# Optimization experiments

Hardware: AMD Instinct MI355X
Metric: run time of the kernel (lower is better)

The kernel has to match this reference:

```python
import jax, jax.numpy as jnp
import numpy as np

NUM_EXPERTS = 256
TOP_K = 8
N_GROUP = 8
TOPK_GROUP = 4
ROUTED_SCALING = 2.5
HIDDEN = 7168
TOKENS = 16384


def setup_inputs() -> dict:
    key = jax.random.key(0)
    k1, k2, k3 = jax.random.split(key, 3)
    hidden_states = jax.random.normal(k1, (TOKENS, HIDDEN), dtype=jnp.float32)
    weight = jax.random.normal(k2, (NUM_EXPERTS, HIDDEN), dtype=jnp.float32) * 0.02
    e_score_correction_bias = jax.random.normal(k3, (NUM_EXPERTS,), dtype=jnp.float32) * 0.1
    return {
        "hidden_states": hidden_states,
        "weight": weight,
        "e_score_correction_bias": e_score_correction_bias,
    }


def reference(hidden_states, weight, e_score_correction_bias):
    T = hidden_states.shape[0]
    experts_per_group = NUM_EXPERTS // N_GROUP
    # Router logits: [T, num_experts]
    router_logits = jnp.einsum("th,eh->te", hidden_states.astype(jnp.float32), weight)
    scores = jax.nn.sigmoid(router_logits)
    scores_for_choice = scores + e_score_correction_bias  # broadcast over tokens
    # ---- group-limited top-k selection (noaux_tc) ----
    scores_grouped = scores_for_choice.reshape(T, N_GROUP, experts_per_group)
    group_top2, _ = jax.lax.top_k(scores_grouped, 2)           # [T, n_group, 2]
    group_scores = group_top2.sum(axis=-1)                      # [T, n_group]
    _, group_indices = jax.lax.top_k(group_scores, TOPK_GROUP)  # [T, topk_group]
    group_mask = jax.nn.one_hot(group_indices, N_GROUP, dtype=scores.dtype).max(axis=1)  # [T, n_group]
    expert_mask = jnp.broadcast_to(group_mask[:, :, None], (T, N_GROUP, experts_per_group)).reshape(T, NUM_EXPERTS)
    masked_scores = scores_for_choice * expert_mask
    # ---- final expert top-k ----
    _, selected_experts = jax.lax.top_k(masked_scores, TOP_K)   # [T, top_k]
    routing_weights = jnp.take_along_axis(scores, selected_experts, axis=-1)
    # norm_topk_prob
    routing_weights = routing_weights / (routing_weights.sum(axis=-1, keepdims=True) + 1e-20)
    routing_weights = routing_weights * ROUTED_SCALING
    return routing_weights, selected_experts
```

## Files before the change

kernel.cpp:

```cpp
#include <hip/hip_runtime.h>
#include <math.h>
#include <stdint.h>

#define TOKENS 16384
#define HIDDEN 7168
#define NE     256
#define NGROUP 8
#define GSIZE  32
#define TOPKG  4
#define TOPK   8

#define KSPLIT 2
#define TM     64
#define BK     32
#define KC_TOTAL (HIDDEN / BK)
#define KC_SLICE (KC_TOTAL / KSPLIT)

#define WPLANES_BYTES ((size_t)KC_TOTAL * 32 * 1024)

typedef _Float16 half8 __attribute__((ext_vector_type(8)));
typedef float    floatx4 __attribute__((ext_vector_type(4)));
typedef unsigned int u32;
#define GAS __attribute__((address_space(1)))
#define LAS __attribute__((address_space(3)))

__global__ void prep_w(const float* __restrict__ W, _Float16* __restrict__ wp) {
    const int c = blockIdx.x * 128 + threadIdx.x;
    const int e = blockIdx.y;
    const float* src = W + (size_t)e * HIDDEN + c * 8;
    float4 v0 = *(const float4*)src;
    float4 v1 = *(const float4*)(src + 4);
    float xv[8] = {v0.x, v0.y, v0.z, v0.w, v1.x, v1.y, v1.z, v1.w};
    half8 h, l;
    #pragma unroll
    for (int j = 0; j < 8; j++) {
        _Float16 hh = (_Float16)xv[j];
        h[j] = hh;
        l[j] = (_Float16)((xv[j] - (float)hh) * 2048.0f);
    }
    const int kc = c >> 2;
    const int g  = c & 3;
    const int lane = g * 16 + (e & 15);
    const int et   = e >> 4;
    const size_t base = (size_t)kc * 16384 + (size_t)et * 512 + (size_t)lane * 8;
    *(half8*)(wp + base)        = h;
    *(half8*)(wp + base + 8192) = l;
}

__global__ __launch_bounds__(256, 2)
void gemm_kernel(const float* __restrict__ X, const _Float16* __restrict__ wp,
                 float* __restrict__ partial) {
    __shared__ __align__(16) _Float16 smem[20480];

    const int tid  = threadIdx.x;
    const int b    = blockIdx.x;
    const int tb   = b >> 1;
    const int ks   = b & 1;
    const int t0   = tb * TM;

    const int w    = tid >> 6;
    const int lane = tid & 63;

    const int at = tid >> 2;
    const int ac = tid & 3;
    const int awoff = (at >> 4) * 512 + (ac * 16 + (at & 15)) * 8;
    const float* Xrow = X + (size_t)(t0 + at) * HIDDEN + ks * (HIDDEN / KSPLIT) + ac * 8;

    const char* wbase = (const char*)wp + (size_t)ks * KC_SLICE * 32768;

    floatx4 acc0[4][4], acc1[4][4];
    #pragma unroll
    for (int i = 0; i < 4; i++)
        #pragma unroll
        for (int j = 0; j < 4; j++) {
            acc0[i][j] = (floatx4){0.f, 0.f, 0.f, 0.f};
            acc1[i][j] = (floatx4){0.f, 0.f, 0.f, 0.f};
        }

    float4 v0 = *(const float4*)Xrow;
    float4 v1 = *(const float4*)(Xrow + 4);

    for (int i = 0; i < KC_SLICE; i++) {
        __syncthreads();

        {
            float xv[8] = {v0.x, v0.y, v0.z, v0.w, v1.x, v1.y, v1.z, v1.w};
            half8 ahh, ahl;
            #pragma unroll
            for (int j = 0; j < 8; j++) {
                _Float16 hh = (_Float16)xv[j];
                ahh[j] = hh;
                ahl[j] = (_Float16)((xv[j] - (float)hh) * 2048.0f);
            }
            *(half8*)(smem + awoff)        = ahh;
            *(half8*)(smem + 2048 + awoff) = ahl;
        }

        {
            const char* wsrc = wbase + (size_t)i * 32768;
            char* bdst = (char*)(smem + 4096);
            #pragma unroll
            for (int q = 0; q < 8; q++) {
                const int o = (tid + 256 * q) * 16;
                __builtin_amdgcn_global_load_lds((GAS const u32*)(wsrc + o),
                                                 (LAS u32*)(bdst + o), 16, 0, 0);
            }
        }

        __syncthreads();

        if (i + 1 < KC_SLICE) {
            const float* xp = Xrow + (size_t)(i + 1) * BK;
            v0 = *(const float4*)xp;
            v1 = *(const float4*)(xp + 4);
        }

        const _Float16* Bb = smem + 4096 + w * 2048;
        half8 bh[4], bl[4];
        #pragma unroll
        for (int et = 0; et < 4; et++) {
            bh[et] = *(const half8*)(Bb + et * 512 + lane * 8);
            bl[et] = *(const half8*)(Bb + 8192 + et * 512 + lane * 8);
        }
        #pragma unroll
        for (int mt = 0; mt < 4; mt++) {
            half8 ah = *(const half8*)(smem + mt * 512 + lane * 8);
            half8 al = *(const half8*)(smem + 2048 + mt * 512 + lane * 8);
            #pragma unroll
            for (int et = 0; et < 4; et++)
                acc0[mt][et] = __builtin_amdgcn_mfma_f32_16x16x32_f16(ah, bh[et], acc0[mt][et], 0, 0, 0);
            #pragma unroll
            for (int et = 0; et < 4; et++)
                acc1[mt][et] = __builtin_amdgcn_mfma_f32_16x16x32_f16(ah, bl[et], acc1[mt][et], 0, 0, 0);
            #pragma unroll
            for (int et = 0; et < 4; et++)
                acc1[mt][et] = __builtin_amdgcn_mfma_f32_16x16x32_f16(al, bh[et], acc1[mt][et], 0, 0, 0);
        }
    }

    float* P = partial + (size_t)ks * TOKENS * NE;
    const float inv = 1.0f / 2048.0f;
    #pragma unroll
    for (int mt = 0; mt < 4; mt++)
        #pragma unroll
        for (int et = 0; et < 4; et++) {
            floatx4 r = acc0[mt][et] + acc1[mt][et] * inv;
            const int col = w * 64 + 16 * et + (lane & 15);
            const int row = t0 + 16 * mt + (lane >> 4) * 4;
            #pragma unroll
            for (int rr = 0; rr < 4; rr++)
                P[(size_t)(row + rr) * NE + col] = r[rr];
        }
}

__global__ __launch_bounds__(256)
void select_kernel(const float* __restrict__ partial, const float* __restrict__ bias,
                   float* __restrict__ out) {
    __shared__ float sfc[32][257];
    const int tid = threadIdx.x;
    const int t0  = blockIdx.x * 32;
    const float* P0 = partial;
    const float* P1 = partial + (size_t)TOKENS * NE;

    for (int idx = tid; idx < 32 * NE; idx += 256) {
        const int t = idx >> 8;
        const int e = idx & 255;
        const size_t g = (size_t)(t0 + t) * NE + e;
        const float logit = P0[g] + P1[g];
        const float sig = 1.0f / (1.0f + expf(-logit));
        sfc[t][e] = sig + bias[e];
    }
    __syncthreads();

    if (tid < 32) {
        float* s = sfc[tid];
        float gs[NGROUP];
        #pragma unroll
        for (int g = 0; g < NGROUP; g++) {
            float m1 = -INFINITY, m2 = -INFINITY;
            for (int x = 0; x < GSIZE; x++) {
                const float v = s[g * GSIZE + x];
                if (v > m1) { m2 = m1; m1 = v; }
                else if (v > m2) { m2 = v; }
            }
            gs[g] = m1 + m2;
        }
        bool gsel[NGROUP] = {false,false,false,false,false,false,false,false};
        for (int r = 0; r < TOPKG; r++) {
            int bi = 0; float bv = -INFINITY;
            for (int g = 0; g < NGROUP; g++)
                if (!gsel[g] && gs[g] > bv) { bv = gs[g]; bi = g; }
            gsel[bi] = true;
        }
        int sel[TOPK]; float wgt[TOPK]; float sum = 0.f;
        for (int r = 0; r < TOPK; r++) {
            int bi = 0; float bv = -INFINITY;
            for (int e = 0; e < NE; e++) {
                const float sv = s[e];
                const float v = (sv == -INFINITY) ? -INFINITY
                               : (gsel[e >> 5] ? sv : 0.0f);
                if (v > bv) { bv = v; bi = e; }
            }
            sel[r] = bi;
            wgt[r] = s[bi] - bias[bi];
            s[bi]  = -INFINITY;
            sum += wgt[r];
        }
        const float scale = 2.5f / (sum + 1e-20f);
        const int gt = t0 + tid;
        #pragma unroll
        for (int r = 0; r < TOPK; r++) {
            out[(size_t)gt * TOPK + r] = wgt[r] * scale;
            out[(size_t)TOKENS * TOPK + (size_t)gt * TOPK + r] = (float)sel[r];
        }
    }
}

extern "C" void kernel_launch(void* const* d_in, const int* in_sizes, int n_in,
                              void* d_out, int out_size, void* d_ws, size_t ws_size,
                              hipStream_t stream) {
    const float* X  = (const float*)d_in[0];
    const float* W  = (const float*)d_in[1];
    const float* eb = (const float*)d_in[2];
    float* out = (float*)d_out;

    _Float16* wp   = (_Float16*)d_ws;
    float* partial = (float*)((char*)d_ws + WPLANES_BYTES);

    hipLaunchKernelGGL(prep_w, dim3(7, 256), dim3(128), 0, stream, W, wp);
    hipLaunchKernelGGL(gemm_kernel, dim3(TOKENS / TM * KSPLIT), dim3(256), 0, stream, X, wp, partial);
    hipLaunchKernelGGL(select_kernel, dim3(TOKENS / 32), dim3(256), 0, stream, partial, eb, out);
}
```

Baseline: 784.3 us.

## Double-buffer weight tiles, raise K-split to 4, warp-parallel routing selection

The GEMM now double-buffers the weight tiles in LDS, prefetching the next K chunk with global_load_lds while the current one is computed, and uses raw barriers with explicit waitcnt. KSPLIT doubles to 4, giving more blocks per token tile, and LDS grows to hold two weight buffers. The select kernel is rewritten so each wavefront handles one token, using shuffle reductions for group top-2, group ranking and the top-8 experts, in place of a single serial thread per token. The cost is more partial-sum traffic, larger LDS per block (which may limit occupancy), and hand-written waitcnt logic that must stay correct.

```diff
diff --git a/kernel.cpp b/kernel.cpp
--- a/kernel.cpp
+++ b/kernel.cpp
@@ -10,7 +10,7 @@
 #define TOPKG  4
 #define TOPK   8
 
-#define KSPLIT 2
+#define KSPLIT 4
 #define TM     64
 #define BK     32
 #define KC_TOTAL (HIDDEN / BK)
@@ -50,12 +50,12 @@
 __global__ __launch_bounds__(256, 2)
 void gemm_kernel(const float* __restrict__ X, const _Float16* __restrict__ wp,
                  float* __restrict__ partial) {
-    __shared__ __align__(16) _Float16 smem[20480];
+    __shared__ __align__(16) _Float16 smem[36864];
 
     const int tid  = threadIdx.x;
     const int b    = blockIdx.x;
-    const int tb   = b >> 1;
-    const int ks   = b & 1;
+    const int tb   = b >> 2;
+    const int ks   = b & 3;
     const int t0   = tb * TM;
 
     const int w    = tid >> 6;
@@ -77,11 +77,34 @@
             acc1[i][j] = (floatx4){0.f, 0.f, 0.f, 0.f};
         }
 
+    {
+        const char* wsrc = wbase;
+        char* bdst = (char*)(smem + 4096);
+        #pragma unroll
+        for (int q = 0; q < 8; q++) {
+            const int o = (tid + 256 * q) * 16;
+            __builtin_amdgcn_global_load_lds((GAS const u32*)(wsrc + o),
+                                             (LAS u32*)(bdst + o), 16, 0, 0);
+        }
+    }
     float4 v0 = *(const float4*)Xrow;
     float4 v1 = *(const float4*)(Xrow + 4);
 
     for (int i = 0; i < KC_SLICE; i++) {
-        __syncthreads();
+        const int cur = i & 1;
+
+        asm volatile("s_barrier" ::: "memory");
+
+        if (i + 1 < KC_SLICE) {
+            const char* wsrc = wbase + (size_t)(i + 1) * 32768;
+            char* bdst = (char*)(smem + 4096 + (cur ^ 1) * 16384);
+            #pragma unroll
+            for (int q = 0; q < 8; q++) {
+                const int o = (tid + 256 * q) * 16;
+                __builtin_amdgcn_global_load_lds((GAS const u32*)(wsrc + o),
+                                                 (LAS u32*)(bdst + o), 16, 0, 0);
+            }
+        }
 
         {
             float xv[8] = {v0.x, v0.y, v0.z, v0.w, v1.x, v1.y, v1.z, v1.w};
@@ -96,26 +119,20 @@
             *(half8*)(smem + 2048 + awoff) = ahl;
         }
 
-        {
-            const char* wsrc = wbase + (size_t)i * 32768;
-            char* bdst = (char*)(smem + 4096);
-            #pragma unroll
-            for (int q = 0; q < 8; q++) {
-                const int o = (tid + 256 * q) * 16;
-                __builtin_amdgcn_global_load_lds((GAS const u32*)(wsrc + o),
-                                                 (LAS u32*)(bdst + o), 16, 0, 0);
-            }
-        }
-
-        __syncthreads();
-
         if (i + 1 < KC_SLICE) {
+            asm volatile("s_waitcnt vmcnt(8) lgkmcnt(0)" ::: "memory");
+            __builtin_amdgcn_sched_barrier(0);
             const float* xp = Xrow + (size_t)(i + 1) * BK;
             v0 = *(const float4*)xp;
             v1 = *(const float4*)(xp + 4);
-        }
-
-        const _Float16* Bb = smem + 4096 + w * 2048;
+        } else {
+            asm volatile("s_waitcnt vmcnt(0) lgkmcnt(0)" ::: "memory");
+            __builtin_amdgcn_sched_barrier(0);
+        }
+
+        asm volatile("s_barrier" ::: "memory");
+
+        const _Float16* Bb = smem + 4096 + cur * 16384 + w * 2048;
         half8 bh[4], bl[4];
         #pragma unroll
         for (int et = 0; et < 4; et++) {
@@ -156,62 +173,85 @@
 __global__ __launch_bounds__(256)
 void select_kernel(const float* __restrict__ partial, const float* __restrict__ bias,
                    float* __restrict__ out) {
-    __shared__ float sfc[32][257];
-    const int tid = threadIdx.x;
-    const int t0  = blockIdx.x * 32;
-    const float* P0 = partial;
-    const float* P1 = partial + (size_t)TOKENS * NE;
-
-    for (int idx = tid; idx < 32 * NE; idx += 256) {
-        const int t = idx >> 8;
-        const int e = idx & 255;
-        const size_t g = (size_t)(t0 + t) * NE + e;
-        const float logit = P0[g] + P1[g];
-        const float sig = 1.0f / (1.0f + expf(-logit));
-        sfc[t][e] = sig + bias[e];
-    }
-    __syncthreads();
-
-    if (tid < 32) {
-        float* s = sfc[tid];
-        float gs[NGROUP];
-        #pragma unroll
-        for (int g = 0; g < NGROUP; g++) {
-            float m1 = -INFINITY, m2 = -INFINITY;
-            for (int x = 0; x < GSIZE; x++) {
-                const float v = s[g * GSIZE + x];
-                if (v > m1) { m2 = m1; m1 = v; }
-                else if (v > m2) { m2 = v; }
-            }
-            gs[g] = m1 + m2;
-        }
-        bool gsel[NGROUP] = {false,false,false,false,false,false,false,false};
-        for (int r = 0; r < TOPKG; r++) {
-            int bi = 0; float bv = -INFINITY;
-            for (int g = 0; g < NGROUP; g++)
-                if (!gsel[g] && gs[g] > bv) { bv = gs[g]; bi = g; }
-            gsel[bi] = true;
-        }
-        int sel[TOPK]; float wgt[TOPK]; float sum = 0.f;
+    const int lane = threadIdx.x & 63;
+    const int t    = blockIdx.x * 4 + (threadIdx.x >> 6);
+    const int e0   = lane * 4;
+
+    float lg[4] = {0.f, 0.f, 0.f, 0.f};
+    #pragma unroll
+    for (int s = 0; s < KSPLIT; s++) {
+        float4 p = *(const float4*)(partial + ((size_t)s * TOKENS + t) * NE + e0);
+        lg[0] += p.x; lg[1] += p.y; lg[2] += p.z; lg[3] += p.w;
+    }
+    float4 b4 = *(const float4*)(bias + e0);
+    const float bb[4] = {b4.x, b4.y, b4.z, b4.w};
+
+    float sig[4], sfc[4];
+    #pragma unroll
+    for (int j = 0; j < 4; j++) {
+        sig[j] = 1.0f / (1.0f + expf(-lg[j]));
+        sfc[j] = sig[j] + bb[j];
+    }
+
+    float m1 = sfc[0], m2 = -INFINITY;
+    #pragma unroll
+    for (int j = 1; j < 4; j++) {
+        if (sfc[j] > m1)      { m2 = m1; m1 = sfc[j]; }
+        else if (sfc[j] > m2) { m2 = sfc[j]; }
+    }
+    #pragma unroll
+    for (int d = 1; d < 8; d <<= 1) {
+        float o1 = __shfl_xor(m1, d);
+        float o2 = __shfl_xor(m2, d);
+        float hi = fmaxf(m1, o1);
+        float lo = fmaxf(fminf(m1, o1), fmaxf(m2, o2));
+        m1 = hi; m2 = lo;
+    }
+    const float gscore = m1 + m2;
+    const int mygroup = lane >> 3;
+
+    int rank = 0;
+    #pragma unroll
+    for (int g = 0; g < 8; g++) {
+        float gs = __shfl(gscore, g * 8);
+        rank += (gs > gscore) || (gs == gscore && g < mygroup);
+    }
+    const bool keep = (rank < TOPKG);
+
+    float cand[4];
+    #pragma unroll
+    for (int j = 0; j < 4; j++) cand[j] = keep ? sfc[j] : 0.0f;
+
+    float wr[TOPK]; int er[TOPK]; float wsum = 0.f;
+    #pragma unroll
+    for (int r = 0; r < TOPK; r++) {
+        float bv = cand[0]; int bj = 0;
+        #pragma unroll
+        for (int j = 1; j < 4; j++) if (cand[j] > bv) { bv = cand[j]; bj = j; }
+        int be = e0 + bj;
+        #pragma unroll
+        for (int d = 1; d < 64; d <<= 1) {
+            float ov = __shfl_xor(bv, d);
+            int   oe = __shfl_xor(be, d);
+            if (ov > bv || (ov == bv && oe < be)) { bv = ov; be = oe; }
+        }
+        const int ol = be >> 2, oj = be & 3;
+        float osig = (oj == 0) ? sig[0] : (oj == 1) ? sig[1] : (oj == 2) ? sig[2] : sig[3];
+        float wv = __shfl(osig, ol);
+        wr[r] = wv; er[r] = be; wsum += wv;
+        const bool own = (ol == lane);
+        cand[0] = (own && oj == 0) ? -INFINITY : cand[0];
+        cand[1] = (own && oj == 1) ? -INFINITY : cand[1];
+        cand[2] = (own && oj == 2) ? -INFINITY : cand[2];
+        cand[3] = (own && oj == 3) ? -INFINITY : cand[3];
+    }
+
+    const float scale = 2.5f / (wsum + 1e-20f);
+    if (lane == 0) {
+        #pragma unroll
         for (int r = 0; r < TOPK; r++) {
-            int bi = 0; float bv = -INFINITY;
-            for (int e = 0; e < NE; e++) {
-                const float sv = s[e];
-                const float v = (sv == -INFINITY) ? -INFINITY
-                               : (gsel[e >> 5] ? sv : 0.0f);
-                if (v > bv) { bv = v; bi = e; }
-            }
-            sel[r] = bi;
-            wgt[r] = s[bi] - bias[bi];
-            s[bi]  = -INFINITY;
-            sum += wgt[r];
-        }
-        const float scale = 2.5f / (sum + 1e-20f);
-        const int gt = t0 + tid;
-        #pragma unroll
-        for (int r = 0; r < TOPK; r++) {
-            out[(size_t)gt * TOPK + r] = wgt[r] * scale;
-            out[(size_t)TOKENS * TOPK + (size_t)gt * TOPK + r] = (float)sel[r];
+            out[(size_t)t * TOPK + r] = wr[r] * scale;
+            out[(size_t)TOKENS * TOPK + (size_t)t * TOPK + r] = (float)er[r];
         }
     }
 }
@@ -229,5 +269,5 @@
 
     hipLaunchKernelGGL(prep_w, dim3(7, 256), dim3(128), 0, stream, W, wp);
     hipLaunchKernelGGL(gemm_kernel, dim3(TOKENS / TM * KSPLIT), dim3(256), 0, stream, X, wp, partial);
-    hipLaunchKernelGGL(select_kernel, dim3(TOKENS / 32), dim3(256), 0, stream, partial, eb, out);
-}
+    hipLaunchKernelGGL(select_kernel, dim3(TOKENS / 4), dim3(256), 0, stream, partial, eb, out);
+}
```

Measured after the change: 727.1 us. -7.3%, faster.
